# Kernel optimization log

Measured on AMD Instinct MI355X. Metric: run time of the kernel, lower is better.

## Reference

```python
import jax, jax.numpy as jnp
import numpy as np


def setup_inputs() -> dict:
    key = jax.random.key(0)
    k1, k2, k3 = jax.random.split(key, 3)
    B, T, I, H, D = 32, 1024, 1024, 16, 64
    x = jax.random.normal(k1, (B, T, I), dtype=jnp.float32)
    kv_kernel = jax.random.normal(k2, (I, H, D, 2), dtype=jnp.float32) * (1.0 / np.sqrt(I))
    q_kernel = jax.random.normal(k3, (H, D), dtype=jnp.float32) * (1.0 / np.sqrt(D))
    return {"x": x, "kv_kernel": kv_kernel, "q_kernel": q_kernel}


def _attention_rnn(x, kv_kernel, q_kernel):
    # x: [B,T,I]; kv_kernel: [I,H,D,2]; q_kernel: [H,D]
    B, T, _ = x.shape
    H, D = q_kernel.shape
    # Projection + silu activation, done once for all timesteps (same math as per-step einsum)
    kv = jnp.einsum('bti,ihdk->bthdk', x, kv_kernel)
    kv = jax.nn.silu(kv)
    k = kv[..., 0]  # [B,T,H,D]
    v = kv[..., 1]  # [B,T,H,D]
    # Per-step attention score s_t = <q_h, k_th>
    s = jnp.einsum('hd,bthd->bth', q_kernel, k)  # [B,T,H]

    # Keras RNN zero-initialized states: num [B,H,D], den [B,H], max [B,H]
    init = (
        jnp.zeros((B, H, D), x.dtype),
        jnp.zeros((B, H), x.dtype),
        jnp.zeros((B, H), x.dtype),
    )

    def step(carry, inp):
        num, den, pmax = carry
        s_t, v_t = inp  # [B,H], [B,H,D]
        cmax = jnp.maximum(pmax, s_t)
        exp_max_diff = jnp.exp(pmax - cmax)
        sm = jnp.exp(s_t - cmax)
        den_n = sm + den * exp_max_diff
        num_n = v_t * sm[..., None] + num * exp_max_diff[..., None]
        h = num_n / den_n[..., None]          # [B,H,D]
        o = jnp.sum(h, axis=-2)               # concat_heads=False -> sum over heads: [B,D]
        return (num_n, den_n, cmax), o

    # scan over time (leading axis)
    _, outs = jax.lax.scan(step, init, (jnp.swapaxes(s, 0, 1), jnp.swapaxes(v, 0, 1)))
    return jnp.swapaxes(outs, 0, 1)  # [B,T,D]


def reference(x, kv_kernel, q_kernel):
    return _attention_rnn(x, kv_kernel, q_kernel)
```

## Files before the change

kernel.cpp:

```cpp
#include <hip/hip_runtime.h>
#include <hip/hip_bf16.h>

#define B_ 32
#define T_ 1024
#define H_ 16
#define D_ 64
#define M_ (B_*T_)
#define N_ (H_*D_*2)
#define K_ 1024
#define CHUNKS 16
#define CLEN (T_/CHUNKS)

typedef __bf16 bf16x8 __attribute__((ext_vector_type(8)));
typedef float  f32x4  __attribute__((ext_vector_type(4)));
typedef unsigned short u16x8 __attribute__((ext_vector_type(8)));

__device__ __forceinline__ float bf2f(unsigned short u){
  union{ float f; unsigned int i; } c; c.i = ((unsigned int)u) << 16; return c.f;
}
__device__ __forceinline__ unsigned short f2bf(float f){
  union{ float f; unsigned int i; } c; c.f = f;
  unsigned int r = (c.i + 0x7FFFu + ((c.i >> 16) & 1u)) >> 16;
  return (unsigned short)r;
}
__device__ __forceinline__ float silu(float x){ return x / (1.0f + __expf(-x)); }
__device__ __forceinline__ float frcp(float x){
  float r; asm("v_rcp_f32 %0, %1" : "=v"(r) : "v"(x)); return r;
}

__device__ __forceinline__ void gload16(const void* g, void* l){
  __builtin_amdgcn_global_load_lds(
      (const __attribute__((address_space(1))) void*)g,
      (__attribute__((address_space(3))) void*)l, 16, 0, 0);
}

#define BAR()   __builtin_amdgcn_s_barrier()
#define LGKM0() asm volatile("s_waitcnt lgkmcnt(0)" ::: "memory")
#define VM4()   asm volatile("s_waitcnt vmcnt(4)" ::: "memory")
#define VM0()   asm volatile("s_waitcnt vmcnt(0)" ::: "memory")

__global__ __launch_bounds__(256) void cvt_xw(const float* __restrict__ x,
                                              unsigned short* __restrict__ xb,
                                              const float* __restrict__ w,
                                              unsigned short* __restrict__ wt){
  __shared__ unsigned short tile[64][65];
  if(blockIdx.x < 2048){
    int i = (blockIdx.x * 256 + threadIdx.x) * 8;
    int stride = 2048 * 256 * 8;
    int n = M_ * K_;
    for(; i < n; i += stride){
      float4 v0 = *(const float4*)(x + i);
      float4 v1 = *(const float4*)(x + i + 4);
      u16x8 o;
      o[0]=f2bf(v0.x); o[1]=f2bf(v0.y); o[2]=f2bf(v0.z); o[3]=f2bf(v0.w);
      o[4]=f2bf(v1.x); o[5]=f2bf(v1.y); o[6]=f2bf(v1.z); o[7]=f2bf(v1.w);
      *(u16x8*)(xb + i) = o;
    }
  } else {
    int blk = blockIdx.x - 2048;
    int kt = (blk & 15) * 64, nt = (blk >> 4) * 64;
    int t = threadIdx.x, tn = t & 63, tk4 = t >> 6;
    #pragma unroll
    for(int r = 0; r < 16; ++r){
      int kl = r * 4 + tk4;
      tile[tn][kl] = f2bf(w[(kt + kl) * N_ + nt + tn]);
    }
    __syncthreads();
    #pragma unroll
    for(int r = 0; r < 16; ++r){
      int nl = r * 4 + tk4;
      int n  = nt + nl;
      int np = (n & ~127) | ((n & 1) << 6) | ((n >> 1) & 63);
      wt[(size_t)np * K_ + kt + tn] = tile[nl][tn];
    }
  }
}

__global__ __launch_bounds__(512, 2) void gemm8(
    const unsigned short* __restrict__ xb,
    const unsigned short* __restrict__ wt,
    const float*  __restrict__ q,
    unsigned short* __restrict__ vout,
    float* __restrict__ s)
{
  __shared__ __align__(16) char lds[131072];

  const int t = threadIdx.x, lane = t & 63, wid = t >> 6;
  const int wr = wid >> 2, wc = wid & 3;
  const int l15 = lane & 15, l4 = lane >> 4;

  const int id  = blockIdx.y * gridDim.x + blockIdx.x;
  const int swz = (id & 7) * 128 + (id >> 3);
  const int bx = swz & 127, by = swz >> 7;
  const int brow = bx * 256, bcol = by * 256;

  f32x4 acc[8][4] = {};
  bf16x8 af[8], b0[4], b1[4];

  const int swl   = l15 & 7;
  const int aoff0 = l15 * 128 + (((0 + l4) ^ swl) << 4);
  const int aoff1 = l15 * 128 + (((4 + l4) ^ swl) << 4);

  auto stage = [&](int buf, int op, int half, const unsigned short* src,
                   int rowbase, int kt){
    char* base = lds + buf * 65536 + op * 32768 + half * 16384;
    #pragma unroll
    for(int L = 0; L < 2; ++L){
      int idx = L * 512 + t;
      int r = idx >> 3, ss = idx & 7;
      gload16(src + (size_t)(rowbase + half * 128 + r) * K_
                  + kt * 64 + ((ss ^ (r & 7)) << 3),
              base + idx * 16);
    }
  };
  auto rdA = [&](int buf, int miBase){
    const char* base = lds + buf * 65536 + wr * 16384;
    #pragma unroll
    for(int m = 0; m < 4; ++m){
      af[m*2+0] = *(const bf16x8*)(base + (miBase + m) * 2048 + aoff0);
      af[m*2+1] = *(const bf16x8*)(base + (miBase + m) * 2048 + aoff1);
    }
  };
  auto rdB = [&](int buf, int niBase, bf16x8 (&dst)[4]){
    const char* base = lds + buf * 65536 + 32768 + (wc >> 1) * 16384 + (wc & 1) * 8192;
    #pragma unroll
    for(int n = 0; n < 2; ++n){
      dst[n*2+0] = *(const bf16x8*)(base + (niBase + n) * 2048 + aoff0);
      dst[n*2+1] = *(const bf16x8*)(base + (niBase + n) * 2048 + aoff1);
    }
  };
  auto mmaq = [&](int miBase, bf16x8 (&bb)[4], int niBase){
    __builtin_amdgcn_s_setprio(1);
    #pragma unroll
    for(int m = 0; m < 4; ++m)
      #pragma unroll
      for(int n = 0; n < 2; ++n)
        #pragma unroll
        for(int k = 0; k < 2; ++k)
          acc[miBase+m][niBase+n] = __builtin_amdgcn_mfma_f32_16x16x32_bf16(
              af[m*2+k], bb[n*2+k], acc[miBase+m][niBase+n], 0, 0, 0);
    __builtin_amdgcn_s_setprio(0);
  };

  stage(0,0,0, xb, brow, 0); stage(0,0,1, xb, brow, 0);
  stage(0,1,0, wt, bcol, 0); stage(0,1,1, wt, bcol, 0);
  stage(1,1,0, wt, bcol, 1); stage(1,1,1, wt, bcol, 1);
  VM4(); BAR();

  for(int i = 0; i < 7; ++i){
    const int t1 = 2*i + 1;
    const int t2 = 2*i + 2;
    const int t3 = 2*i + 3;
    rdA(0,0); rdB(0,0,b0); stage(1,0,0, xb, brow, t1);
    BAR(); LGKM0(); mmaq(0,b0,0); BAR();
    rdB(0,2,b1); stage(1,0,1, xb, brow, t1);
    BAR(); LGKM0(); mmaq(0,b1,2); BAR();
    rdA(0,4); stage(0,1,0, wt, bcol, t2);
    BAR(); LGKM0(); mmaq(4,b1,2); BAR();
    stage(0,1,1, wt, bcol, t2); VM4();
    BAR(); mmaq(4,b0,0); BAR();
    rdA(1,0); rdB(1,0,b0); stage(0,0,0, xb, brow, t2);
    BAR(); LGKM0(); mmaq(0,b0,0); BAR();
    rdB(1,2,b1); stage(0,0,1, xb, brow, t2);
    BAR(); LGKM0(); mmaq(0,b1,2); BAR();
    rdA(1,4); stage(1,1,0, wt, bcol, t3);
    BAR(); LGKM0(); mmaq(4,b1,2); BAR();
    stage(1,1,1, wt, bcol, t3); VM4();
    BAR(); mmaq(4,b0,0); BAR();
  }
  rdA(0,0); rdB(0,0,b0); stage(1,0,0, xb, brow, 15);
  BAR(); LGKM0(); mmaq(0,b0,0); BAR();
  rdB(0,2,b1); stage(1,0,1, xb, brow, 15);
  BAR(); LGKM0(); mmaq(0,b1,2); BAR();
  rdA(0,4);
  BAR(); LGKM0(); mmaq(4,b1,2); BAR();
  VM0();
  BAR(); mmaq(4,b0,0); BAR();
  rdA(1,0); rdB(1,0,b0);
  BAR(); LGKM0(); mmaq(0,b0,0); BAR();
  rdB(1,2,b1);
  BAR(); LGKM0(); mmaq(0,b1,2); BAR();
  rdA(1,4);
  BAR(); LGKM0(); mmaq(4,b1,2); BAR();
  mmaq(4,b0,0);

  const int hh = by * 2 + (wc >> 1);
  if(wc & 1){
    #pragma unroll
    for(int mi = 0; mi < 8; ++mi)
      #pragma unroll
      for(int r = 0; r < 4; ++r){
        const int gm = brow + wr*128 + mi*16 + l4*4 + r;
        const int bb = gm >> 10, tt = gm & (T_-1);
        unsigned short* vrow = vout + (((size_t)bb*H_ + hh)*T_ + tt)*D_;
        #pragma unroll
        for(int ni = 0; ni < 4; ++ni)
          vrow[ni*16 + l15] = f2bf(silu(acc[mi][ni][r]));
      }
  } else {
    float qv[4];
    #pragma unroll
    for(int ni = 0; ni < 4; ++ni) qv[ni] = q[hh*D_ + ni*16 + l15];
    #pragma unroll
    for(int mi = 0; mi < 8; ++mi)
      #pragma unroll
      for(int r = 0; r < 4; ++r){
        float sc = 0.f;
        #pragma unroll
        for(int ni = 0; ni < 4; ++ni) sc += qv[ni] * silu(acc[mi][ni][r]);
        sc += __shfl_xor(sc, 1); sc += __shfl_xor(sc, 2);
        sc += __shfl_xor(sc, 4); sc += __shfl_xor(sc, 8);
        if(l15 == 0){
          const int gm = brow + wr*128 + mi*16 + l4*4 + r;
          s[(size_t)gm * H_ + hh] = sc;
        }
      }
  }
}

__global__ __launch_bounds__(256) void scan1(
    const unsigned short* __restrict__ v, const float* __restrict__ s,
    float* __restrict__ snum, float* __restrict__ sden, float* __restrict__ smax)
{
  __shared__ float sst[CLEN][H_+1];
  const int blk = blockIdx.x;
  const int c = blk & (CHUNKS-1), b = blk / CHUNKS;
  const int t = threadIdx.x, lane = t & 63, w = t >> 6, h0 = w * 4;

  const float* sbase = s + ((size_t)b*T_ + c*CLEN) * H_;
  for(int i = t; i < CLEN*H_; i += 256) sst[i >> 4][i & 15] = sbase[i];
  __syncthreads();

  float mfix[4];
  #pragma unroll
  for(int j = 0; j < 4; ++j){
    float mm = sst[lane][h0 + j];
    mm = fmaxf(mm, __shfl_xor(mm, 1));  mm = fmaxf(mm, __shfl_xor(mm, 2));
    mm = fmaxf(mm, __shfl_xor(mm, 4));  mm = fmaxf(mm, __shfl_xor(mm, 8));
    mm = fmaxf(mm, __shfl_xor(mm, 16)); mm = fmaxf(mm, __shfl_xor(mm, 32));
    mfix[j] = mm;
  }

  float den[4] = {0.f,0.f,0.f,0.f}, num[4] = {0.f,0.f,0.f,0.f};
  const unsigned short* vb = v + (((size_t)b*H_ + h0)*T_ + c*CLEN)*D_;
  for(int tt = 0; tt < CLEN; ++tt){
    #pragma unroll
    for(int j = 0; j < 4; ++j){
      float p  = __expf(sst[tt][h0 + j] - mfix[j]);
      float vt = bf2f(vb[(size_t)j*T_*D_ + tt*D_ + lane]);
      den[j] += p;
      num[j] += p * vt;
    }
  }
  #pragma unroll
  for(int j = 0; j < 4; ++j){
    int sb = (b*H_ + h0 + j)*CHUNKS + c;
    snum[(size_t)sb*64 + lane] = num[j];
    if(lane == 0){ sden[sb] = den[j]; smax[sb] = mfix[j]; }
  }
}

__global__ __launch_bounds__(256) void scan2h(
    const unsigned short* __restrict__ v, const float* __restrict__ s,
    const float* __restrict__ snum, const float* __restrict__ sden,
    const float* __restrict__ smax, float* __restrict__ out)
{
  __shared__ float sst[CLEN][H_+1];
  __shared__ float oacc[4][CLEN][68];
  const int blk = blockIdx.x;
  const int c = blk & (CHUNKS-1), b = blk / CHUNKS;
  const int t = threadIdx.x, lane = t & 63, w = t >> 6, h0 = w * 4;

  const float* sbase = s + ((size_t)b*T_ + c*CLEN) * H_;
  for(int i = t; i < CLEN*H_; i += 256) sst[i >> 4][i & 15] = sbase[i];
  __syncthreads();

  float num[4], den[4], m[4];
  #pragma unroll
  for(int j = 0; j < 4; ++j){ num[j] = 0.f; den[j] = 0.f; m[j] = -3.0e38f; }

  for(int cc = 0; cc < c; ++cc){
    #pragma unroll
    for(int j = 0; j < 4; ++j){
      int sb = (b*H_ + h0 + j)*CHUNKS + cc;
      float m2 = smax[sb], d2 = sden[sb], n2 = snum[(size_t)sb*64 + lane];
      float cm = fmaxf(m[j], m2);
      float e1 = __expf(m[j]-cm), e2 = __expf(m2-cm);
      den[j] = den[j]*e1 + d2*e2;
      num[j] = num[j]*e1 + n2*e2;
      m[j] = cm;
    }
  }

  float mfix[4];
  #pragma unroll
  for(int j = 0; j < 4; ++j){
    int sb = (b*H_ + h0 + j)*CHUNKS + c;
    mfix[j] = fmaxf(m[j], smax[sb]);
    float sc = __expf(m[j] - mfix[j]);
    den[j] *= sc;
    num[j] *= sc;
  }

  const unsigned short* vb = v + (((size_t)b*H_ + h0)*T_ + c*CLEN)*D_;
  for(int tt = 0; tt < CLEN; ++tt){
    float o = 0.f;
    #pragma unroll
    for(int j = 0; j < 4; ++j){
      float p  = __expf(sst[tt][h0 + j] - mfix[j]);
      float vt = bf2f(vb[(size_t)j*T_*D_ + tt*D_ + lane]);
      den[j] += p;
      num[j] += p * vt;
      o += num[j] * frcp(den[j]);
    }
    oacc[w][tt][lane] = o;
  }
  __syncthreads();

  {
    int tt = t >> 2, db = (t & 3) * 16;
    float* ob = out + ((size_t)b*T_ + c*CLEN + tt) * D_ + db;
    #pragma unroll
    for(int qd = 0; qd < 4; ++qd){
      f32x4 a0 = *(const f32x4*)&oacc[0][tt][db + qd*4];
      f32x4 a1 = *(const f32x4*)&oacc[1][tt][db + qd*4];
      f32x4 a2 = *(const f32x4*)&oacc[2][tt][db + qd*4];
      f32x4 a3 = *(const f32x4*)&oacc[3][tt][db + qd*4];
      f32x4 r = (a0 + a1) + (a2 + a3);
      *(f32x4*)(ob + qd*4) = r;
    }
  }
}

extern "C" void kernel_launch(void* const* d_in, const int* in_sizes, int n_in,
                              void* d_out, int out_size, void* d_ws, size_t ws_size,
                              hipStream_t stream){
  (void)in_sizes; (void)n_in; (void)out_size; (void)ws_size;
  const float* x = (const float*)d_in[0];
  const float* w = (const float*)d_in[1];
  const float* q = (const float*)d_in[2];
  float* out = (float*)d_out;
  char* ws = (char*)d_ws;

  unsigned short* wt   = (unsigned short*)(ws);
  unsigned short* xb   = (unsigned short*)(ws + (4u  << 20));
  unsigned short* vbuf = (unsigned short*)(ws + (68u << 20));
  float* s    = (float*)(ws + (132u << 20));
  float* snum = (float*)(ws + (8u  << 20));
  float* sden = (float*)(ws + (12u << 20));
  float* smax = (float*)(ws + (12u << 20) + (1u << 16));

  cvt_xw<<<2048 + 512, 256, 0, stream>>>(x, xb, w, wt);
  gemm8<<<dim3(M_/256, N_/256), 512, 0, stream>>>(xb, wt, q, vbuf, s);
  scan1<<<B_*CHUNKS, 256, 0, stream>>>(vbuf, s, snum, sden, smax);
  scan2h<<<B_*CHUNKS, 256, 0, stream>>>(vbuf, s, snum, sden, smax, out);
}
```

Measured before the change: 234.8 us.

## Make GEMM blocks persistent over four row tiles with cross-tile prefetch

The GEMM launch drops from 1024 blocks to 256, and each block now computes four consecutive 256-row tiles for one column tile. The loads for the next tile's first K-steps are issued during the current tile's tail, so the pipeline does not drain and refill between tiles. The aim is to cut the cost of block launch and prologue/epilogue, and to keep the weight columns resident in cache. In exchange there are fewer blocks (256 on a device with many CUs), which can hurt load balance, and the epilogue stores no longer overlap with other blocks' compute.

Result: slower. 367.0 us (+56.3%).

```diff
diff --git a/kernel.cpp b/kernel.cpp
--- a/kernel.cpp
+++ b/kernel.cpp
@@ -89,12 +89,12 @@
   const int wr = wid >> 2, wc = wid & 3;
   const int l15 = lane & 15, l4 = lane >> 4;
 
-  const int id  = blockIdx.y * gridDim.x + blockIdx.x;
-  const int swz = (id & 7) * 128 + (id >> 3);
-  const int bx = swz & 127, by = swz >> 7;
-  const int brow = bx * 256, bcol = by * 256;
-
-  f32x4 acc[8][4] = {};
+  const int p = blockIdx.x;
+  const int by = p & 7, bxg = p >> 3;
+  const int bcol = by * 256;
+  const int hh = by * 2 + (wc >> 1);
+
+  f32x4 acc[8][4];
   bf16x8 af[8], b0[4], b1[4];
 
   const int swl   = l15 & 7;
@@ -142,79 +142,106 @@
     __builtin_amdgcn_s_setprio(0);
   };
 
-  stage(0,0,0, xb, brow, 0); stage(0,0,1, xb, brow, 0);
-  stage(0,1,0, wt, bcol, 0); stage(0,1,1, wt, bcol, 0);
-  stage(1,1,0, wt, bcol, 1); stage(1,1,1, wt, bcol, 1);
-  VM4(); BAR();
-
-  for(int i = 0; i < 7; ++i){
-    const int t1 = 2*i + 1;
-    const int t2 = 2*i + 2;
-    const int t3 = 2*i + 3;
-    rdA(0,0); rdB(0,0,b0); stage(1,0,0, xb, brow, t1);
+  {
+    const int brow0 = bxg * 1024;
+    stage(0,0,0, xb, brow0, 0); stage(0,0,1, xb, brow0, 0);
+    stage(0,1,0, wt, bcol, 0);  stage(0,1,1, wt, bcol, 0);
+    stage(1,1,0, wt, bcol, 1);  stage(1,1,1, wt, bcol, 1);
+    VM4(); BAR();
+  }
+
+  for(int tt = 0; tt < 4; ++tt){
+    const int brow  = (bxg*4 + tt) * 256;
+    const int nbrow = brow + 256;
+    #pragma unroll
+    for(int mi = 0; mi < 8; ++mi)
+      #pragma unroll
+      for(int ni = 0; ni < 4; ++ni)
+        acc[mi][ni] = (f32x4){0.f,0.f,0.f,0.f};
+
+    for(int i = 0; i < 7; ++i){
+      const int t1 = 2*i + 1;
+      const int t2 = 2*i + 2;
+      const int t3 = 2*i + 3;
+      rdA(0,0); rdB(0,0,b0); stage(1,0,0, xb, brow, t1);
+      BAR(); LGKM0(); mmaq(0,b0,0); BAR();
+      rdB(0,2,b1); stage(1,0,1, xb, brow, t1);
+      BAR(); LGKM0(); mmaq(0,b1,2); BAR();
+      rdA(0,4); stage(0,1,0, wt, bcol, t2);
+      BAR(); LGKM0(); mmaq(4,b1,2); BAR();
+      stage(0,1,1, wt, bcol, t2); VM4();
+      BAR(); mmaq(4,b0,0); BAR();
+      rdA(1,0); rdB(1,0,b0); stage(0,0,0, xb, brow, t2);
+      BAR(); LGKM0(); mmaq(0,b0,0); BAR();
+      rdB(1,2,b1); stage(0,0,1, xb, brow, t2);
+      BAR(); LGKM0(); mmaq(0,b1,2); BAR();
+      rdA(1,4); stage(1,1,0, wt, bcol, t3);
+      BAR(); LGKM0(); mmaq(4,b1,2); BAR();
+      stage(1,1,1, wt, bcol, t3); VM4();
+      BAR(); mmaq(4,b0,0); BAR();
+    }
+    rdA(0,0); rdB(0,0,b0); stage(1,0,0, xb, brow, 15);
     BAR(); LGKM0(); mmaq(0,b0,0); BAR();
-    rdB(0,2,b1); stage(1,0,1, xb, brow, t1);
+    rdB(0,2,b1); stage(1,0,1, xb, brow, 15);
     BAR(); LGKM0(); mmaq(0,b1,2); BAR();
-    rdA(0,4); stage(0,1,0, wt, bcol, t2);
-    BAR(); LGKM0(); mmaq(4,b1,2); BAR();
-    stage(0,1,1, wt, bcol, t2); VM4();
-    BAR(); mmaq(4,b0,0); BAR();
-    rdA(1,0); rdB(1,0,b0); stage(0,0,0, xb, brow, t2);
-    BAR(); LGKM0(); mmaq(0,b0,0); BAR();
-    rdB(1,2,b1); stage(0,0,1, xb, brow, t2);
-    BAR(); LGKM0(); mmaq(0,b1,2); BAR();
-    rdA(1,4); stage(1,1,0, wt, bcol, t3);
-    BAR(); LGKM0(); mmaq(4,b1,2); BAR();
-    stage(1,1,1, wt, bcol, t3); VM4();
-    BAR(); mmaq(4,b0,0); BAR();
-  }
-  rdA(0,0); rdB(0,0,b0); stage(1,0,0, xb, brow, 15);
-  BAR(); LGKM0(); mmaq(0,b0,0); BAR();
-  rdB(0,2,b1); stage(1,0,1, xb, brow, 15);
-  BAR(); LGKM0(); mmaq(0,b1,2); BAR();
-  rdA(0,4);
-  BAR(); LGKM0(); mmaq(4,b1,2); BAR();
-  VM0();
-  BAR(); mmaq(4,b0,0); BAR();
-  rdA(1,0); rdB(1,0,b0);
-  BAR(); LGKM0(); mmaq(0,b0,0); BAR();
-  rdB(1,2,b1);
-  BAR(); LGKM0(); mmaq(0,b1,2); BAR();
-  rdA(1,4);
-  BAR(); LGKM0(); mmaq(4,b1,2); BAR();
-  mmaq(4,b0,0);
-
-  const int hh = by * 2 + (wc >> 1);
-  if(wc & 1){
-    #pragma unroll
-    for(int mi = 0; mi < 8; ++mi)
-      #pragma unroll
-      for(int r = 0; r < 4; ++r){
-        const int gm = brow + wr*128 + mi*16 + l4*4 + r;
-        const int bb = gm >> 10, tt = gm & (T_-1);
-        unsigned short* vrow = vout + (((size_t)bb*H_ + hh)*T_ + tt)*D_;
+    if(tt < 3){
+      rdA(0,4); stage(0,1,0, wt, bcol, 0);
+      BAR(); LGKM0(); mmaq(4,b1,2); BAR();
+      stage(0,1,1, wt, bcol, 0); VM4();
+      BAR(); mmaq(4,b0,0); BAR();
+      rdA(1,0); rdB(1,0,b0); stage(0,0,0, xb, nbrow, 0);
+      BAR(); LGKM0(); mmaq(0,b0,0); BAR();
+      rdB(1,2,b1); stage(0,0,1, xb, nbrow, 0);
+      BAR(); LGKM0(); mmaq(0,b1,2); BAR();
+      rdA(1,4); stage(1,1,0, wt, bcol, 1);
+      BAR(); LGKM0(); mmaq(4,b1,2); BAR();
+      stage(1,1,1, wt, bcol, 1); VM4();
+      BAR(); mmaq(4,b0,0); BAR();
+    } else {
+      rdA(0,4);
+      BAR(); LGKM0(); mmaq(4,b1,2); BAR();
+      VM0();
+      BAR(); mmaq(4,b0,0); BAR();
+      rdA(1,0); rdB(1,0,b0);
+      BAR(); LGKM0(); mmaq(0,b0,0); BAR();
+      rdB(1,2,b1);
+      BAR(); LGKM0(); mmaq(0,b1,2); BAR();
+      rdA(1,4);
+      BAR(); LGKM0(); mmaq(4,b1,2); BAR();
+      mmaq(4,b0,0);
+    }
+
+    if(wc & 1){
+      #pragma unroll
+      for(int mi = 0; mi < 8; ++mi)
         #pragma unroll
-        for(int ni = 0; ni < 4; ++ni)
-          vrow[ni*16 + l15] = f2bf(silu(acc[mi][ni][r]));
-      }
-  } else {
-    float qv[4];
-    #pragma unroll
-    for(int ni = 0; ni < 4; ++ni) qv[ni] = q[hh*D_ + ni*16 + l15];
-    #pragma unroll
-    for(int mi = 0; mi < 8; ++mi)
-      #pragma unroll
-      for(int r = 0; r < 4; ++r){
-        float sc = 0.f;
+        for(int r = 0; r < 4; ++r){
+          const int gm = brow + wr*128 + mi*16 + l4*4 + r;
+          const int bb = gm >> 10, ttm = gm & (T_-1);
+          unsigned short* vrow = vout + (((size_t)bb*H_ + hh)*T_ + ttm)*D_;
+          #pragma unroll
+          for(int ni = 0; ni < 4; ++ni)
+            vrow[ni*16 + l15] = f2bf(silu(acc[mi][ni][r]));
+        }
+    } else {
+      float qv[4];
+      #pragma unroll
+      for(int ni = 0; ni < 4; ++ni) qv[ni] = q[hh*D_ + ni*16 + l15];
+      #pragma unroll
+      for(int mi = 0; mi < 8; ++mi)
         #pragma unroll
-        for(int ni = 0; ni < 4; ++ni) sc += qv[ni] * silu(acc[mi][ni][r]);
-        sc += __shfl_xor(sc, 1); sc += __shfl_xor(sc, 2);
-        sc += __shfl_xor(sc, 4); sc += __shfl_xor(sc, 8);
-        if(l15 == 0){
-          const int gm = brow + wr*128 + mi*16 + l4*4 + r;
-          s[(size_t)gm * H_ + hh] = sc;
+        for(int r = 0; r < 4; ++r){
+          float sc = 0.f;
+          #pragma unroll
+          for(int ni = 0; ni < 4; ++ni) sc += qv[ni] * silu(acc[mi][ni][r]);
+          sc += __shfl_xor(sc, 1); sc += __shfl_xor(sc, 2);
+          sc += __shfl_xor(sc, 4); sc += __shfl_xor(sc, 8);
+          if(l15 == 0){
+            const int gm = brow + wr*128 + mi*16 + l4*4 + r;
+            s[(size_t)gm * H_ + hh] = sc;
+          }
         }
-      }
+    }
   }
 }
 
@@ -351,7 +378,7 @@
   float* smax = (float*)(ws + (12u << 20) + (1u << 16));
 
   cvt_xw<<<2048 + 512, 256, 0, stream>>>(x, xb, w, wt);
-  gemm8<<<dim3(M_/256, N_/256), 512, 0, stream>>>(xb, wt, q, vbuf, s);
+  gemm8<<<256, 512, 0, stream>>>(xb, wt, q, vbuf, s);
   scan1<<<B_*CHUNKS, 256, 0, stream>>>(vbuf, s, snum, sden, smax);
   scan2h<<<B_*CHUNKS, 256, 0, stream>>>(vbuf, s, snum, sden, smax, out);
 }
```
